# Optimization experiments

Measured on AMD Instinct MI355X. Metric: run time of the kernel, lower is better.

The kernel has to match this reference:

```python
import jax, jax.numpy as jnp
import numpy as np

B, L, P = 65536, 512, 96
E_LIN, E = 14, 16
FFT = 512
TEMP = 0.07
K = 2
EPS = 1e-5


def setup_inputs() -> dict:
    key = jax.random.key(0)
    k0, k1, k2 = jax.random.split(key, 3)
    x = jax.random.normal(k0, (B, L), dtype=jnp.float32)
    Wg = jax.random.normal(k1, (E, FFT // 2), dtype=jnp.float32) * 0.02
    bg = jnp.zeros((E,), dtype=jnp.float32)
    Wr = jax.random.normal(k2, (E_LIN, P, L), dtype=jnp.float32) * 0.02
    br = jnp.zeros((E_LIN, P), dtype=jnp.float32)
    return {"x": x, "Wg": Wg, "bg": bg, "Wr": Wr, "br": br}


def _periodogram(x):
    # x: [B, L] -> normalized power spectrum [B, FFT//2]
    x0 = x - jnp.mean(x, axis=1, keepdims=True)
    dft = jnp.fft.fft(x0, n=FFT, axis=1) / np.float32(np.sqrt(FFT))
    dft = dft[:, : FFT // 2]
    I = dft.real ** 2 + dft.imag ** 2
    s = jnp.sum(I, axis=1, keepdims=True)
    s = jnp.where(s == 0, jnp.ones_like(s), s)
    return I / s


def reference(x, Wg, bg, Wr, br):
    # gating (eval mode: no noise, divide by temperature)
    I = _periodogram(x)                                  # [B, F/2]
    gate = (I @ Wg.T + bg) / TEMP                        # [B, E]
    topv, topi = jax.lax.top_k(gate, K)                  # [B, K]
    gates = jax.nn.softmax(topv, axis=1)                 # [B, K]

    # RLinear experts: RevIN(norm) -> Linear -> RevIN(denorm); stats detached
    mu = jax.lax.stop_gradient(jnp.mean(x, axis=1, keepdims=True))        # [B,1]
    sd = jax.lax.stop_gradient(jnp.sqrt(jnp.var(x, axis=1, keepdims=True) + EPS))
    xn = (x - mu) / sd                                   # [B, L]
    yr = jnp.einsum('bl,epl->bep', xn, Wr) + br          # [B, E_LIN, P]
    yr = yr * sd[:, :, None] + mu[:, :, None]

    mean_out = jnp.broadcast_to(jnp.mean(x, axis=1, keepdims=True), (x.shape[0], P))[:, None, :]
    naive_out = jnp.broadcast_to(x[:, -1:], (x.shape[0], P))[:, None, :]

    eo = jnp.concatenate([yr, mean_out, naive_out], axis=1)   # [B, E, P]
    sel = jnp.take_along_axis(eo, topi[:, :, None], axis=1)   # [B, K, P]
    out = jnp.sum(gates[:, :, None] * sel, axis=1)            # [B, P]
    return out
```

## Files before the change

kernel.cpp:

```cpp
#include <hip/hip_runtime.h>
#include <math.h>

#define NB_B 65536
#define NL   512
#define NP   96
#define NE   16
#define NEL  14
#define NF   256
#define TEMP_INV (1.0f/0.07f)
#define TAU  1e-5f
#define PI_D 3.14159265358979323846
#define MAXCHK 1536

typedef __attribute__((ext_vector_type(8))) short bf16x8;
typedef __attribute__((ext_vector_type(4))) float f32x4;


#define WS_PCNT     0
#define WS_HOLES    16384
#define WS_PBASE    32768
#define WS_FLAGCNT  33792
#define WS_NCHK     33824
#define WS_HOLECNT  33840
#define WS_FLAG     33856
#define WS_SSUM     296000
#define WS_WGT      301376
#define WS_BGT      317760
#define WS_TWD      319872
#define WS_REC      328064
#define WS_HDR      590208
#define WS_RIDX     1638784
#define WS_WRB      1900928
#define WS_DESC     3473792
#define WS_XB16     3480064
#define WS_WRBF     70588928
#define WS_WRBF_END 72161792

__device__ __forceinline__ unsigned short f2bf(float f) {
    unsigned u = __float_as_uint(f);
    unsigned r = (u + 0x7fffu + ((u >> 16) & 1u)) >> 16;
    return (unsigned short)r;
}

__global__ __launch_bounds__(256) void k_prep(
    const float* __restrict__ Wg, const float* __restrict__ bg,
    const float* __restrict__ Wr,
    float* __restrict__ Ssum, float* __restrict__ WgE, float* __restrict__ bgT,
    double2* __restrict__ twd,
    int* __restrict__ pcnt, int* __restrict__ flagcnt, int* __restrict__ holecnt,
    ushort4* __restrict__ Wrb, ushort4* __restrict__ WrbF, int perm)
{
    int g = blockIdx.x * 256 + threadIdx.x;
    {
        ushort4 o = make_ushort4(0, 0, 0, 0);
        if (g < NEL * NP * NL / 4) {
            float4 v;
            if (perm) {
                int row = g >> 7, sq = g & 127;
                int ll = sq >> 1, kb = (sq & 1) * 4;
                const float* wr = Wr + (size_t)row * NL + ll;
                v.x = wr[(kb + 0) * 64]; v.y = wr[(kb + 1) * 64];
                v.z = wr[(kb + 2) * 64]; v.w = wr[(kb + 3) * 64];
            } else {
                v = ((const float4*)Wr)[g];
            }
            o.x = f2bf(v.x); o.y = f2bf(v.y); o.z = f2bf(v.z); o.w = f2bf(v.w);
        }
        Wrb[g] = o;
    }
    if (WrbF) {
        ushort4 o = make_ushort4(0, 0, 0, 0);
        int idx  = g >> 1;
        int lane = idx & 63;
        int idx2 = idx >> 6;
        int nt   = idx2 % 6;
        int idx3 = idx2 / 6;
        int ks   = idx3 & 1;
        int idx4 = idx3 >> 1;
        int kb8  = idx4 & 7;
        int e    = idx4 >> 3;
        if (e < NEL) {
            int p = nt * 16 + (lane & 15);
            int quad = lane >> 4;
            int skb = kb8 * 64 + ks * 32 + quad * 8 + (g & 1) * 4;
            const float* wr = Wr + ((size_t)e * NP + p) * NL;
            float vv[4];
#pragma unroll
            for (int jj = 0; jj < 4; jj++) {
                int sk = skb + jj;
                int ko = perm ? ((sk & 7) * 64 + (sk >> 3)) : sk;
                vv[jj] = wr[ko];
            }
            o.x = f2bf(vv[0]); o.y = f2bf(vv[1]); o.z = f2bf(vv[2]); o.w = f2bf(vv[3]);
        }
        WrbF[g] = o;
    }
    if (g < NEL * NP * 8) {
        int row = g >> 3, seg = g & 7;
        const float4* w = (const float4*)(Wr + (size_t)row * NL + seg * 64);
        float s = 0.f;
#pragma unroll
        for (int i = 0; i < 16; i++) { float4 v = w[i]; s += v.x + v.y + v.z + v.w; }
        s += __shfl_xor(s, 1); s += __shfl_xor(s, 2); s += __shfl_xor(s, 4);
        if (seg == 0) Ssum[row] = s;
    }
    if (g < 4096) {
        int c = g & 3, e = (g >> 2) & 15, f4 = g >> 6;
        WgE[g] = Wg[e * NF + f4 * 4 + c] * TEMP_INV;
    }
    if (g < 512) {
        double a = -2.0 * PI_D * (double)g / 512.0;
        twd[g] = make_double2(cos(a), sin(a));
    }
    if (g < 256) pcnt[g << 4] = 0;
    if (g < NE) bgT[g] = bg[g] * TEMP_INV;
    if (g == 300) *flagcnt = 0;
    if (g == 301) *holecnt = 0;
}

__global__ __launch_bounds__(256) void k_gate(
    const float* __restrict__ x,
    const float4* __restrict__ WgE4, const float* __restrict__ bgT,
    int* __restrict__ rec, float4* __restrict__ hdr,
    int* __restrict__ flaglist, int* __restrict__ flagcnt,
    int* __restrict__ pcnt, unsigned short* __restrict__ xb16)
{
    __shared__ __align__(16) float2 s_z[4][576];
    float* s_Iv = (float*)&s_z[0][0];

    const int t = threadIdx.x;
    const int wv = t >> 6, l = t & 63;
    const int b0 = blockIdx.x * 8 + wv * 2;

    const float th = -6.283185307179586f / 512.0f;
    const float R2 = 0.70710678118654752f;
    float s1, c1; __sincosf((float)l * th, &s1, &c1);
    float s2, c2; __sincosf((float)(2 * l) * th, &s2, &c2);
    float sw0, cw0; __sincosf((float)((l & 31) << 3) * th, &sw0, &cw0);
    float sw1, cw1; __sincosf((float)((l & 15) << 4) * th, &sw1, &cw1);
    float sw2, cw2; __sincosf((float)((l & 7) << 5) * th, &sw2, &cw2);
    float2 tw0[4];
    tw0[0] = make_float2(c1, s1);
    tw0[1] = make_float2(R2 * (c1 + s1), R2 * (s1 - c1));
    tw0[2] = make_float2(s1, -c1);
    tw0[3] = make_float2(tw0[1].y, -tw0[1].x);
    float2 tw1[2];
    tw1[0] = make_float2(c2, s2);
    tw1[1] = make_float2(s2, -c2);
    const float2 w2 = make_float2(c2 * c2 - s2 * s2, 2.f * c2 * s2);
    float2 wst[5];
    wst[0] = make_float2(cw0, sw0);
    wst[1] = make_float2(cw1, sw1);
    wst[2] = make_float2(cw2, sw2);
    {
        int j2 = l & 3;
        float cc3 = (j2 == 0) ? 1.f : (j2 == 1) ? R2 : (j2 == 2) ? 0.f : -R2;
        float ss3 = (j2 == 0) ? 0.f : (j2 == 2) ? -1.f : -R2;
        wst[3] = make_float2(cc3, ss3);
    }
    wst[4] = (l & 1) ? make_float2(0.f, -1.f) : make_float2(1.f, 0.f);

    const float* xa = x + (size_t)b0 * NL;
    const float* xb = xa + NL;
    float xr[8], xi[8];
#pragma unroll
    for (int k = 0; k < 8; k++) { xr[k] = xa[k * 64 + l]; xi[k] = xb[k * 64 + l]; }
    const float last_a = __shfl(xr[7], 63);
    const float last_b = __shfl(xi[7], 63);

    if (xb16) {
        unsigned pa_[4], pb_[4];
#pragma unroll
        for (int j = 0; j < 4; j++) {
            asm("v_cvt_pk_bf16_f32 %0, %1, %2" : "=v"(pa_[j]) : "v"(xr[2 * j]), "v"(xr[2 * j + 1]));
            asm("v_cvt_pk_bf16_f32 %0, %1, %2" : "=v"(pb_[j]) : "v"(xi[2 * j]), "v"(xi[2 * j + 1]));
        }
        *(uint4*)(xb16 + (size_t)b0 * NL + l * 8)       = *(uint4*)pa_;
        *(uint4*)(xb16 + (size_t)(b0 + 1) * NL + l * 8) = *(uint4*)pb_;
    }

#pragma unroll
    for (int k = 0; k < 4; k++) {
        float2 w = tw0[k];
        float ur = xr[k], ui = xi[k], vr = xr[k + 4], vi = xi[k + 4];
        xr[k] = ur + vr; xi[k] = ui + vi;
        float dr = ur - vr, di = ui - vi;
        xr[k + 4] = dr * w.x - di * w.y; xi[k + 4] = dr * w.y + di * w.x;
    }
    {
        const int kk[4] = {0, 1, 4, 5};
#pragma unroll
        for (int g2 = 0; g2 < 4; g2++) {
            int k = kk[g2];
            float2 w = tw1[k & 1];
            float ur = xr[k], ui = xi[k], vr = xr[k + 2], vi = xi[k + 2];
            xr[k] = ur + vr; xi[k] = ui + vi;
            float dr = ur - vr, di = ui - vi;
            xr[k + 2] = dr * w.x - di * w.y; xi[k + 2] = dr * w.y + di * w.x;
        }
    }
    {
#pragma unroll
        for (int k = 0; k < 8; k += 2) {
            float ur = xr[k], ui = xi[k], vr = xr[k + 1], vi = xi[k + 1];
            xr[k] = ur + vr; xi[k] = ui + vi;
            float dr = ur - vr, di = ui - vi;
            xr[k + 1] = dr * w2.x - di * w2.y; xi[k + 1] = dr * w2.y + di * w2.x;
        }
    }
#pragma unroll
    for (int st = 3; st < 8; st++) {
        const int half = 256 >> st;
        const float2 w = wst[st - 3];
        const bool up = (l & half) != 0;
        const float sg = up ? -1.f : 1.f;
        const float cc = up ? w.x : 1.f;
        const float ss = up ? w.y : 0.f;
#pragma unroll
        for (int k = 0; k < 8; k++) {
            float pr = __shfl_xor(xr[k], half);
            float pi = __shfl_xor(xi[k], half);
            float tr = fmaf(sg, xr[k], pr);
            float ti = fmaf(sg, xi[k], pi);
            xr[k] = tr * cc - ti * ss;
            xi[k] = tr * ss + ti * cc;
        }
    }
    {
        const float sg = (l & 1) ? -1.f : 1.f;
#pragma unroll
        for (int k = 0; k < 8; k++) {
            float pr = __shfl_xor(xr[k], 1);
            float pi = __shfl_xor(xi[k], 1);
            xr[k] = fmaf(sg, xr[k], pr);
            xi[k] = fmaf(sg, xi[k], pi);
        }
    }

#pragma unroll
    for (int k = 0; k < 8; k++) {
        int i = k * 64 + l;
        s_z[wv][i + (i >> 3)] = make_float2(xr[k], xi[k]);
    }

    float Ia[4], Ib[4];
    float psa = 0.f, psb = 0.f;
#pragma unroll
    for (int j = 0; j < 4; j++) {
        int f = (l << 2) | j;
        int i1_ = (int)(__brev((unsigned)f) >> 23);
        int i2_ = (int)(__brev((unsigned)((512 - f) & 511)) >> 23);
        float2 z1 = s_z[wv][i1_ + (i1_ >> 3)];
        float2 z2 = s_z[wv][i2_ + (i2_ >> 3)];
        float pr_ = z1.x + z2.x, qm = z1.y - z2.y;
        float qp = z1.y + z2.y, pm = z1.x - z2.x;
        float va = pr_ * pr_ + qm * qm;
        float vb = qp * qp + pm * pm;
        if (f == 0) { va = 0.f; vb = 0.f; }
        Ia[j] = va; Ib[j] = vb;
        psa += va; psb += vb;
    }
#pragma unroll
    for (int m = 1; m < 64; m <<= 1) {
        psa += __shfl_xor(psa, m); psb += __shfl_xor(psb, m);
    }
    const float psa_raw = psa, psb_raw = psb;
    if (psa == 0.f) psa = 1.f;
    if (psb == 0.f) psb = 1.f;
    const float inv_a = 1.f / psa, inv_b = 1.f / psb;

    const float2 Z0   = s_z[wv][0];
    const float2 Z256 = s_z[wv][1];

    float* wI = s_Iv + wv * 1152;
    const int io = (l << 2) + ((l >> 4) << 2);
    *(float4*)(wI + io)       = make_float4(Ia[0], Ia[1], Ia[2], Ia[3]);
    *(float4*)(wI + 272 + io) = make_float4(Ib[0], Ib[1], Ib[2], Ib[3]);

    const int e16 = l & 15, cq = l >> 4;
    const float bgv = bgT[e16];
    float accA = 0.f, accB = 0.f;
    const float* rA = wI + cq * 68;
    const float* rB = rA + 272;
#pragma unroll 4
    for (int jj = 0; jj < 16; jj++) {
        float4 ia = *(const float4*)(rA + 4 * jj);
        float4 ib = *(const float4*)(rB + 4 * jj);
        float4 w = WgE4[(cq * 16 + jj) * 16 + e16];
        accA += ia.x * w.x + ia.y * w.y + ia.z * w.z + ia.w * w.w;
        accB += ib.x * w.x + ib.y * w.y + ib.z * w.z + ib.w * w.w;
    }
    accA += __shfl_xor(accA, 16); accA += __shfl_xor(accA, 32);
    accB += __shfl_xor(accB, 16); accB += __shfl_xor(accB, 32);

    float v = ((l & 16) ? accB * inv_b : accA * inv_a) + bgv;

    float b0v = v; int b0i = e16;
#pragma unroll
    for (int m = 1; m < 16; m <<= 1) {
        float ov = __shfl_xor(b0v, m); int oi = __shfl_xor(b0i, m);
        if (ov > b0v || (ov == b0v && oi < b0i)) { b0v = ov; b0i = oi; }
    }
    float v1 = (e16 == b0i) ? -1e30f : v;
    float b1v = v1; int b1i = e16;
#pragma unroll
    for (int m = 1; m < 16; m <<= 1) {
        float ov = __shfl_xor(b1v, m); int oi = __shfl_xor(b1i, m);
        if (ov > b1v || (ov == b1v && oi < b1i)) { b1v = ov; b1i = oi; }
    }
    float v2 = (e16 == b1i) ? -1e30f : v1;
    float b2v = v2;
#pragma unroll
    for (int m = 1; m < 16; m <<= 1) {
        float ov = __shfl_xor(b2v, m);
        b2v = fmaxf(b2v, ov);
    }

    if (l == 0 || l == 16) {
        const int r = l >> 4;
        const int b = b0 + r;
        const float mu = (r ? Z0.y : Z0.x) * (1.f / 512.f);
        const float Jv = r ? Z256.y : Z256.x;
        const float ps = r ? psb_raw : psa_raw;
        const float sd = sqrtf((0.5f * ps + Jv * Jv) * (1.f / 262144.f) + 1e-5f);
        const float last = r ? last_b : last_a;
        const float w0 = 1.f / (1.f + expf(b1v - b0v));
        const int pid = b0i * 16 + b1i;
        const int lo = atomicAdd(&pcnt[pid << 4], 1);
        rec[b] = (pid << 24) | lo;
        hdr[b] = make_float4(mu, sd, last, w0);
        if (b1v - b2v < TAU) {
            int pos = atomicAdd(flagcnt, 1);
            flaglist[pos] = b;
        }
    }
}

__global__ __launch_bounds__(256) void k_refine(
    const float* __restrict__ x, const double2* __restrict__ twd,
    const float* __restrict__ Wg, const float* __restrict__ bg,
    int* __restrict__ rec, float4* __restrict__ hdr,
    const int* __restrict__ flaglist, const int* __restrict__ flagcnt,
    int* __restrict__ pcnt, int* __restrict__ holes, int* __restrict__ holecnt)
{
    __shared__ double s_x[512];
    __shared__ double s_I[256];
    __shared__ double s_red[16];
    __shared__ double s_g[16];
    const int nf = *flagcnt;
    const int t = threadIdx.x;
    const int wid = t >> 6, lane = t & 63;
    for (int fi = blockIdx.x; fi < nf; fi += gridDim.x) {
        const int b = flaglist[fi];
        const float* xp = x + (size_t)b * NL;
        double v0 = (double)xp[t], v1 = (double)xp[t + 256];
        double lsum = v0 + v1;
        for (int m = 1; m < 64; m <<= 1) lsum += __shfl_xor(lsum, m);
        if (lane == 0) s_red[wid] = lsum;
        __syncthreads();
        double mu = (s_red[0] + s_red[1] + s_red[2] + s_red[3]) * (1.0 / 512.0);
        s_x[t] = v0 - mu; s_x[t + 256] = v1 - mu;
        __syncthreads();
        double2 w = twd[t];
        double pr = 1.0, pi = 0.0, cr = 0.0, ci = 0.0;
        for (int n = 0; n < 512; n++) {
            double xv = s_x[n];
            cr += xv * pr; ci += xv * pi;
            double t2 = pr * w.x - pi * w.y;
            pi = pr * w.y + pi * w.x;
            pr = t2;
        }
        double I = cr * cr + ci * ci;
        s_I[t] = I;
        double ls = I;
        for (int m = 1; m < 64; m <<= 1) ls += __shfl_xor(ls, m);
        if (lane == 0) s_red[8 + wid] = ls;
        __syncthreads();
        double stot = s_red[8] + s_red[9] + s_red[10] + s_red[11];
        if (stot == 0.0) stot = 1.0;
        if (t < 16) {
            double acc = 0.0;
            const float* wrow = Wg + t * NF;
            for (int f = 0; f < NF; f++) acc += s_I[f] * (double)wrow[f];
            s_g[t] = (acc / stot + (double)bg[t]) * (1.0 / 0.07);
        }
        __syncthreads();
        if (t == 0) {
            double c0 = -1e300, c1 = -1e300; int j0 = 0, j1 = 0;
            for (int i = 0; i < 16; i++) {
                double v = s_g[i];
                if (v > c0) { c1 = c0; j1 = j0; c0 = v; j0 = i; }
                else if (v > c1) { c1 = v; j1 = i; }
            }
            double e1 = exp(c1 - c0);
            float w0f = (float)(1.0 / (1.0 + e1));
            int newpid = j0 * 16 + j1;
            int oldrec = rec[b];
            int oldpid = (int)(((unsigned)oldrec) >> 24);
            if (newpid == oldpid) {
                ((float*)(hdr + b))[3] = w0f;
            } else {
                int pos = atomicAdd(holecnt, 1);
                if (pos < 4096) {
                    int nlo = atomicAdd(&pcnt[newpid << 4], 1);
                    rec[b] = (newpid << 24) | nlo;
                    holes[pos] = oldrec;
                    ((float*)(hdr + b))[3] = w0f;
                }
            }
        }
        __syncthreads();
    }
}

__global__ __launch_bounds__(256) void k_scan(
    const int* __restrict__ pcnt, int* __restrict__ pbase,
    int* __restrict__ desc, int* __restrict__ nchk)
{
    __shared__ int s[256], c[256];
    const int t = threadIdx.x;
    const int n = pcnt[t << 4];
    s[t] = n;
    c[t] = (n + 63) >> 6;
    __syncthreads();
    for (int off = 1; off < 256; off <<= 1) {
        int v1 = (t >= off) ? s[t - off] : 0;
        int v2 = (t >= off) ? c[t - off] : 0;
        __syncthreads();
        s[t] += v1; c[t] += v2;
        __syncthreads();
    }
    int excl = t ? s[t - 1] : 0;
    int cexcl = t ? c[t - 1] : 0;
    pbase[t] = excl;
    int myc = (n + 63) >> 6;
    for (int j = 0; j < myc; j++) desc[cexcl + j] = (t << 16) | j;
    if (t == 255) *nchk = cexcl + myc;
}

__global__ __launch_bounds__(256) void k_scatter(
    const int* __restrict__ rec, const int* __restrict__ pbase,
    int* __restrict__ ridx,
    const int* __restrict__ holes, const int* __restrict__ holecnt)
{
    const int t = threadIdx.x;
    const int b = blockIdx.x * 256 + t;
    unsigned v = (unsigned)rec[b];
    ridx[pbase[v >> 24] + (v & 0xFFFFFF)] = b;
    if (blockIdx.x == 0) {
        int nh = *holecnt; if (nh > 4096) nh = 4096;
        for (int h = t; h < nh; h += 256) {
            unsigned hv = (unsigned)holes[h];
            ridx[pbase[hv >> 24] + (hv & 0xFFFFFF)] = -1;
        }
    }
}

__global__ __launch_bounds__(256) void k_gemm_reg(
    const unsigned short* __restrict__ xb16,
    const unsigned short* __restrict__ WrbF,
    const float* __restrict__ br, const float* __restrict__ Ssum,
    const float4* __restrict__ hdr, float* __restrict__ out,
    const int* __restrict__ pcnt, const int* __restrict__ pbase,
    const int* __restrict__ ridx,
    const int* __restrict__ desc, const int* __restrict__ nchk)
{
    __shared__ int    s_idx[64];
    __shared__ float4 s_hdr[64];
    __shared__ float  s_br[2][96], s_S[2][96];
    if ((int)blockIdx.x >= *nchk) return;
    const int d = desc[blockIdx.x];
    const int pid = d >> 16, cc = d & 0xffff;
    const int n = pcnt[pid << 4];
    const int base = pbase[pid];
    const int i0 = pid >> 4, i1 = pid & 15;
    const int t = threadIdx.x;
    const int lane = t & 63, wv = t >> 6;
    const int quad = lane >> 4, l16 = lane & 15;
    if (t < 96) {
        s_br[0][t] = (i0 < NEL) ? br[i0 * NP + t] : 0.f;
        s_S [0][t] = (i0 < NEL) ? Ssum[i0 * NP + t] : 0.f;
        s_br[1][t] = (i1 < NEL) ? br[i1 * NP + t] : 0.f;
        s_S [1][t] = (i1 < NEL) ? Ssum[i1 * NP + t] : 0.f;
    }
    if (t < 64) {
        int g = cc * 64 + t;
        bool vld = g < n;
        int row = vld ? ridx[base + g] : -1;
        s_idx[t] = row;
        s_hdr[t] = (row >= 0) ? hdr[row] : make_float4(0.f, 0.f, 0.f, 0.f);
    }
    __syncthreads();

    int myrow = s_idx[wv * 16 + l16]; if (myrow < 0) myrow = 0;
    const unsigned short* aP = xb16 + (size_t)myrow * NL + quad * 8;
    const unsigned short* bP[2];
    bP[0] = WrbF + (size_t)i0 * 49152 + lane * 8;
    bP[1] = WrbF + (size_t)i1 * 49152 + lane * 8;

    f32x4 acc[2][6];
#pragma unroll
    for (int ex = 0; ex < 2; ex++)
#pragma unroll
        for (int j = 0; j < 6; j++) acc[ex][j] = (f32x4){0.f, 0.f, 0.f, 0.f};

#pragma unroll
    for (int kb8 = 0; kb8 < 8; kb8++) {
        bf16x8 a0 = *(const bf16x8*)(aP + kb8 * 64);
        bf16x8 a1 = *(const bf16x8*)(aP + kb8 * 64 + 32);
        bf16x8 bfr[2][2][6];
#pragma unroll
        for (int ks = 0; ks < 2; ks++)
#pragma unroll
            for (int ex = 0; ex < 2; ex++)
#pragma unroll
                for (int nt = 0; nt < 6; nt++)
                    bfr[ks][ex][nt] = *(const bf16x8*)(bP[ex] + kb8 * 6144 + ks * 3072 + nt * 512);
#pragma unroll
        for (int ks = 0; ks < 2; ks++)
#pragma unroll
            for (int ex = 0; ex < 2; ex++)
#pragma unroll
                for (int nt = 0; nt < 6; nt++)
                    acc[ex][nt] = __builtin_amdgcn_mfma_f32_16x16x32_bf16(
                        ks ? a1 : a0, bfr[ks][ex][nt], acc[ex][nt], 0, 0, 0);
    }

#pragma unroll
    for (int i = 0; i < 4; i++) {
        int rloc = wv * 16 + quad * 4 + i;
        int row = s_idx[rloc];
        if (row >= 0) {
            float4 h = s_hdr[rloc];
            float mu = h.x, sd = h.y, last = h.z, w0 = h.w, w1 = 1.f - w0;
            float* orow = out + (size_t)row * NP;
#pragma unroll
            for (int nt = 0; nt < 6; nt++) {
                int p = nt * 16 + l16;
                float v0 = (i0 < NEL) ? (mu + s_br[0][p] * sd - mu * s_S[0][p] + acc[0][nt][i])
                                      : (i0 == NEL ? mu : last);
                float v1 = (i1 < NEL) ? (mu + s_br[1][p] * sd - mu * s_S[1][p] + acc[1][nt][i])
                                      : (i1 == NEL ? mu : last);
                orow[p] = w0 * v0 + w1 * v1;
            }
        }
    }
}

template<int XB>
__global__ __launch_bounds__(256) void k_gemm(
    const float* __restrict__ x, const unsigned short* __restrict__ xb16,
    const unsigned short* __restrict__ Wrb,
    const float* __restrict__ br, const float* __restrict__ Ssum,
    const float4* __restrict__ hdr, float* __restrict__ out,
    const int* __restrict__ pcnt, const int* __restrict__ pbase,
    const int* __restrict__ ridx,
    const int* __restrict__ desc, const int* __restrict__ nchk)
{
    __shared__ __align__(16) unsigned short sA[64 * 72];
    __shared__ __align__(16) unsigned short sB[2][96 * 72];
    __shared__ int    s_idx[64];
    __shared__ float4 s_hdr[64];
    __shared__ float  s_br[2][96], s_S[2][96];
    if ((int)blockIdx.x >= *nchk) return;
    const int d = desc[blockIdx.x];
    const int pid = d >> 16, cc = d & 0xffff;
    const int n = pcnt[pid << 4];
    const int base = pbase[pid];
    const int i0 = pid >> 4, i1 = pid & 15;
    const int t = threadIdx.x;
    const int lane = t & 63, wv = t >> 6;
    const int quad = lane >> 4, l16 = lane & 15;
    const int ar = t >> 2, asub = t & 3;
    if (t < 96) {
        s_br[0][t] = (i0 < NEL) ? br[i0 * NP + t] : 0.f;
        s_S [0][t] = (i0 < NEL) ? Ssum[i0 * NP + t] : 0.f;
        s_br[1][t] = (i1 < NEL) ? br[i1 * NP + t] : 0.f;
        s_S [1][t] = (i1 < NEL) ? Ssum[i1 * NP + t] : 0.f;
    }
    if (t < 64) {
        int g = cc * 64 + t;
        bool vld = g < n;
        int row = vld ? ridx[base + g] : -1;
        s_idx[t] = row;
        s_hdr[t] = (row >= 0) ? hdr[row] : make_float4(0.f, 0.f, 0.f, 0.f);
    }
    __syncthreads();

    f32x4 acc[2][6];
#pragma unroll
    for (int ex = 0; ex < 2; ex++)
#pragma unroll
        for (int j = 0; j < 6; j++) acc[ex][j] = (f32x4){0.f, 0.f, 0.f, 0.f};

    int rr = s_idx[ar]; if (rr < 0) rr = 0;

    unsigned boff[6];
    unsigned short* bdst[6];
    const unsigned short* wb[2];
    wb[0] = Wrb + (size_t)i0 * NP * NL;
    wb[1] = Wrb + (size_t)i1 * NP * NL;
    int bex[6];
#pragma unroll
    for (int it = 0; it < 6; it++) {
        int ex = (it >= 3);
        int fl = t + (it - 3 * ex) * 256;
        int p = fl >> 3, kg = fl & 7;
        bex[it] = ex;
        boff[it] = (unsigned)(p * NL + kg * 8);
        bdst[it] = &sB[ex][p * 72 + kg * 8];
    }
    unsigned short* adst = sA + ar * 72 + asub * 16;

    const unsigned short* xrow16 = xb16 + (size_t)rr * NL + asub * 16;
    const float* xrowf = x + (size_t)rr * NL + asub * 16;

    bf16x8 aR[2]; float4 fA[4]; bf16x8 bR[6];

    if constexpr (XB) {
        aR[0] = *(const bf16x8*)(xrow16);
        aR[1] = *(const bf16x8*)(xrow16 + 8);
    } else {
#pragma unroll
        for (int i = 0; i < 4; i++) fA[i] = ((const float4*)xrowf)[i];
    }
#pragma unroll
    for (int it = 0; it < 6; it++) bR[it] = *(const bf16x8*)(wb[bex[it]] + boff[it]);

    for (int kb = 0; kb < NL; kb += 64) {
        if constexpr (XB) {
            *(bf16x8*)adst       = aR[0];
            *(bf16x8*)(adst + 8) = aR[1];
        } else {
            unsigned short tmp[16];
#pragma unroll
            for (int i = 0; i < 4; i++) {
                float4 v = fA[i];
                tmp[i * 4 + 0] = f2bf(v.x); tmp[i * 4 + 1] = f2bf(v.y);
                tmp[i * 4 + 2] = f2bf(v.z); tmp[i * 4 + 3] = f2bf(v.w);
            }
            *(bf16x8*)adst       = *(bf16x8*)tmp;
            *(bf16x8*)(adst + 8) = *(bf16x8*)(tmp + 8);
        }
#pragma unroll
        for (int it = 0; it < 6; it++) *(bf16x8*)bdst[it] = bR[it];
        __syncthreads();

        const int kn = kb + 64;
        if (kn < NL) {
            if constexpr (XB) {
                aR[0] = *(const bf16x8*)(xrow16 + kn);
                aR[1] = *(const bf16x8*)(xrow16 + kn + 8);
            } else {
#pragma unroll
                for (int i = 0; i < 4; i++) fA[i] = ((const float4*)(xrowf + kn))[i];
            }
#pragma unroll
            for (int it = 0; it < 6; it++)
                bR[it] = *(const bf16x8*)(wb[bex[it]] + boff[it] + kn);
        }

#pragma unroll
        for (int ks = 0; ks < 2; ks++) {
            bf16x8 af = *(const bf16x8*)(sA + (wv * 16 + l16) * 72 + ks * 32 + quad * 8);
#pragma unroll
            for (int ex = 0; ex < 2; ex++)
#pragma unroll
                for (int nt = 0; nt < 6; nt++) {
                    bf16x8 bf = *(const bf16x8*)(&sB[ex][(nt * 16 + l16) * 72 + ks * 32 + quad * 8]);
                    acc[ex][nt] = __builtin_amdgcn_mfma_f32_16x16x32_bf16(af, bf, acc[ex][nt], 0, 0, 0);
                }
        }
        __syncthreads();
    }
#pragma unroll
    for (int i = 0; i < 4; i++) {
        int rloc = wv * 16 + quad * 4 + i;
        int row = s_idx[rloc];
        if (row >= 0) {
            float4 h = s_hdr[rloc];
            float mu = h.x, sd = h.y, last = h.z, w0 = h.w, w1 = 1.f - w0;
            float* orow = out + (size_t)row * NP;
#pragma unroll
            for (int nt = 0; nt < 6; nt++) {
                int p = nt * 16 + l16;
                float v0 = (i0 < NEL) ? (mu + s_br[0][p] * sd - mu * s_S[0][p] + acc[0][nt][i])
                                      : (i0 == NEL ? mu : last);
                float v1 = (i1 < NEL) ? (mu + s_br[1][p] * sd - mu * s_S[1][p] + acc[1][nt][i])
                                      : (i1 == NEL ? mu : last);
                orow[p] = w0 * v0 + w1 * v1;
            }
        }
    }
}

extern "C" void kernel_launch(void* const* d_in, const int* in_sizes, int n_in,
                              void* d_out, int out_size, void* d_ws, size_t ws_size,
                              hipStream_t stream)
{
    const float* x  = (const float*)d_in[0];
    const float* Wg = (const float*)d_in[1];
    const float* bg = (const float*)d_in[2];
    const float* Wr = (const float*)d_in[3];
    const float* br = (const float*)d_in[4];
    float* out = (float*)d_out;
    char* ws = (char*)d_ws;

    int*     pcnt     = (int*)(ws + WS_PCNT);
    int*     holes    = (int*)(ws + WS_HOLES);
    int*     pbase    = (int*)(ws + WS_PBASE);
    int*     flagcnt  = (int*)(ws + WS_FLAGCNT);
    int*     nchk     = (int*)(ws + WS_NCHK);
    int*     holecnt  = (int*)(ws + WS_HOLECNT);
    int*     flaglist = (int*)(ws + WS_FLAG);
    float*   Ssum     = (float*)(ws + WS_SSUM);
    float*   WgE      = (float*)(ws + WS_WGT);
    float*   bgT      = (float*)(ws + WS_BGT);
    double2* twd      = (double2*)(ws + WS_TWD);
    int*     rec      = (int*)(ws + WS_REC);
    float4*  hdr      = (float4*)(ws + WS_HDR);
    int*     ridx     = (int*)(ws + WS_RIDX);
    unsigned short* Wrb = (unsigned short*)(ws + WS_WRB);
    int*     desc     = (int*)(ws + WS_DESC);

    const int use_xb  = (ws_size >= (size_t)WS_WRBF);
    const int use_xb2 = (ws_size >= (size_t)WS_WRBF_END);
    unsigned short* xb16 = use_xb  ? (unsigned short*)(ws + WS_XB16) : (unsigned short*)0;
    unsigned short* WrbF = use_xb2 ? (unsigned short*)(ws + WS_WRBF) : (unsigned short*)0;

    k_prep<<<dim3(768), dim3(256), 0, stream>>>(Wg, bg, Wr, Ssum, WgE, bgT, twd,
                                                pcnt, flagcnt, holecnt,
                                                (ushort4*)Wrb, (ushort4*)WrbF, use_xb);
    k_gate<<<dim3(NB_B / 8), dim3(256), 0, stream>>>(x, (const float4*)WgE, bgT,
                                                     rec, hdr, flaglist, flagcnt, pcnt, xb16);
    k_refine<<<dim3(512), dim3(256), 0, stream>>>(x, twd, Wg, bg, rec, hdr,
                                                  flaglist, flagcnt, pcnt, holes, holecnt);
    k_scan<<<dim3(1), dim3(256), 0, stream>>>(pcnt, pbase, desc, nchk);
    k_scatter<<<dim3(NB_B / 256), dim3(256), 0, stream>>>(rec, pbase, ridx, holes, holecnt);
    if (use_xb2)
        k_gemm_reg<<<dim3(MAXCHK), dim3(256), 0, stream>>>(xb16, WrbF, br, Ssum, hdr, out,
                                                           pcnt, pbase, ridx, desc, nchk);
    else if (use_xb)
        k_gemm<1><<<dim3(MAXCHK), dim3(256), 0, stream>>>(x, xb16, Wrb, br, Ssum, hdr, out,
                                                          pcnt, pbase, ridx, desc, nchk);
    else
        k_gemm<0><<<dim3(MAXCHK), dim3(256), 0, stream>>>(x, xb16, Wrb, br, Ssum, hdr, out,
                                                          pcnt, pbase, ridx, desc, nchk);
}
```

Measured before the change: 311.9 us.

## Stage expert weights through double-buffered LDS and split gate launch

Drops the fragment-ordered WrbF weight copy. The GEMM kernel now stages both experts' bf16 weight tiles through a double-buffered shared-memory buffer (stride 68) and reads A fragments directly from the bf16 copy of x in global memory, prefetching the next K block while MFMAs run. The gate kernel gains a launch-bounds occupancy hint and is split into two half-grid launches using a block offset. The aim is to cut per-block global weight traffic and remove the weight-permutation work in prep, at the cost of extra LDS use and one barrier per K step.

```diff
diff --git a/kernel.cpp b/kernel.cpp
--- a/kernel.cpp
+++ b/kernel.cpp
@@ -30,11 +30,10 @@
 #define WS_REC      328064
 #define WS_HDR      590208
 #define WS_RIDX     1638784
-#define WS_WRB      1900928
-#define WS_DESC     3473792
-#define WS_XB16     3480064
-#define WS_WRBF     70588928
-#define WS_WRBF_END 72161792
+#define WS_WRB      1933696
+#define WS_DESC     3506560
+#define WS_XB16     3512704
+#define WS_XB16_END 70621568
 
 __device__ __forceinline__ unsigned short f2bf(float f) {
     unsigned u = __float_as_uint(f);
@@ -48,7 +47,7 @@
     float* __restrict__ Ssum, float* __restrict__ WgE, float* __restrict__ bgT,
     double2* __restrict__ twd,
     int* __restrict__ pcnt, int* __restrict__ flagcnt, int* __restrict__ holecnt,
-    ushort4* __restrict__ Wrb, ushort4* __restrict__ WrbF, int perm)
+    ushort4* __restrict__ Wrb, int perm)
 {
     int g = blockIdx.x * 256 + threadIdx.x;
     {
@@ -68,33 +67,6 @@
         }
         Wrb[g] = o;
     }
-    if (WrbF) {
-        ushort4 o = make_ushort4(0, 0, 0, 0);
-        int idx  = g >> 1;
-        int lane = idx & 63;
-        int idx2 = idx >> 6;
-        int nt   = idx2 % 6;
-        int idx3 = idx2 / 6;
-        int ks   = idx3 & 1;
-        int idx4 = idx3 >> 1;
-        int kb8  = idx4 & 7;
-        int e    = idx4 >> 3;
-        if (e < NEL) {
-            int p = nt * 16 + (lane & 15);
-            int quad = lane >> 4;
-            int skb = kb8 * 64 + ks * 32 + quad * 8 + (g & 1) * 4;
-            const float* wr = Wr + ((size_t)e * NP + p) * NL;
-            float vv[4];
-#pragma unroll
-            for (int jj = 0; jj < 4; jj++) {
-                int sk = skb + jj;
-                int ko = perm ? ((sk & 7) * 64 + (sk >> 3)) : sk;
-                vv[jj] = wr[ko];
-            }
-            o.x = f2bf(vv[0]); o.y = f2bf(vv[1]); o.z = f2bf(vv[2]); o.w = f2bf(vv[3]);
-        }
-        WrbF[g] = o;
-    }
     if (g < NEL * NP * 8) {
         int row = g >> 3, seg = g & 7;
         const float4* w = (const float4*)(Wr + (size_t)row * NL + seg * 64);
@@ -118,19 +90,19 @@
     if (g == 301) *holecnt = 0;
 }
 
-__global__ __launch_bounds__(256) void k_gate(
+__global__ __launch_bounds__(256, 4) void k_gate(
     const float* __restrict__ x,
     const float4* __restrict__ WgE4, const float* __restrict__ bgT,
     int* __restrict__ rec, float4* __restrict__ hdr,
     int* __restrict__ flaglist, int* __restrict__ flagcnt,
-    int* __restrict__ pcnt, unsigned short* __restrict__ xb16)
+    int* __restrict__ pcnt, unsigned short* __restrict__ xb16, int bofs)
 {
     __shared__ __align__(16) float2 s_z[4][576];
     float* s_Iv = (float*)&s_z[0][0];
 
     const int t = threadIdx.x;
     const int wv = t >> 6, l = t & 63;
-    const int b0 = blockIdx.x * 8 + wv * 2;
+    const int b0 = (bofs + blockIdx.x) * 8 + wv * 2;
 
     const float th = -6.283185307179586f / 512.0f;
     const float R2 = 0.70710678118654752f;
@@ -456,15 +428,16 @@
     }
 }
 
-__global__ __launch_bounds__(256) void k_gemm_reg(
+__global__ __launch_bounds__(256) void k_gemm2(
     const unsigned short* __restrict__ xb16,
-    const unsigned short* __restrict__ WrbF,
+    const unsigned short* __restrict__ Wrb,
     const float* __restrict__ br, const float* __restrict__ Ssum,
     const float4* __restrict__ hdr, float* __restrict__ out,
     const int* __restrict__ pcnt, const int* __restrict__ pbase,
     const int* __restrict__ ridx,
     const int* __restrict__ desc, const int* __restrict__ nchk)
 {
+    __shared__ __align__(16) unsigned short sB[2][2][96 * 68];
     __shared__ int    s_idx[64];
     __shared__ float4 s_hdr[64];
     __shared__ float  s_br[2][96], s_S[2][96];
@@ -490,13 +463,30 @@
         s_idx[t] = row;
         s_hdr[t] = (row >= 0) ? hdr[row] : make_float4(0.f, 0.f, 0.f, 0.f);
     }
+
+    const unsigned short* wb[2];
+    wb[0] = Wrb + (size_t)i0 * NP * NL;
+    wb[1] = Wrb + (size_t)i1 * NP * NL;
+    unsigned boff[6]; int bpos[6], bex[6];
+#pragma unroll
+    for (int it = 0; it < 6; it++) {
+        int ex = (it >= 3);
+        int fl = t + (it - 3 * ex) * 256;
+        int p = fl >> 3, kg = fl & 7;
+        bex[it] = ex;
+        boff[it] = (unsigned)(p * NL + kg * 8);
+        bpos[it] = p * 68 + kg * 8;
+    }
+
+    bf16x8 bR[6];
+#pragma unroll
+    for (int it = 0; it < 6; it++) bR[it] = *(const bf16x8*)(wb[bex[it]] + boff[it]);
+#pragma unroll
+    for (int it = 0; it < 6; it++) *(bf16x8*)(&sB[0][bex[it]][bpos[it]]) = bR[it];
     __syncthreads();
 
-    int myrow = s_idx[wv * 16 + l16]; if (myrow < 0) myrow = 0;
-    const unsigned short* aP = xb16 + (size_t)myrow * NL + quad * 8;
-    const unsigned short* bP[2];
-    bP[0] = WrbF + (size_t)i0 * 49152 + lane * 8;
-    bP[1] = WrbF + (size_t)i1 * 49152 + lane * 8;
+    int arow = s_idx[wv * 16 + l16]; if (arow < 0) arow = 0;
+    const unsigned short* aP = xb16 + (size_t)arow * NL + quad * 8;
 
     f32x4 acc[2][6];
 #pragma unroll
@@ -504,26 +494,37 @@
 #pragma unroll
         for (int j = 0; j < 6; j++) acc[ex][j] = (f32x4){0.f, 0.f, 0.f, 0.f};
 
-#pragma unroll
-    for (int kb8 = 0; kb8 < 8; kb8++) {
-        bf16x8 a0 = *(const bf16x8*)(aP + kb8 * 64);
-        bf16x8 a1 = *(const bf16x8*)(aP + kb8 * 64 + 32);
-        bf16x8 bfr[2][2][6];
+    bf16x8 a0 = *(const bf16x8*)(aP);
+    bf16x8 a1 = *(const bf16x8*)(aP + 32);
+
+    int cb = 0;
+    for (int kb = 0; kb < NL; kb += 64) {
+        const int kn = kb + 64;
+        bf16x8 an0, an1;
+        if (kn < NL) {
+#pragma unroll
+            for (int it = 0; it < 6; it++)
+                bR[it] = *(const bf16x8*)(wb[bex[it]] + boff[it] + kn);
+            an0 = *(const bf16x8*)(aP + kn);
+            an1 = *(const bf16x8*)(aP + kn + 32);
+        }
 #pragma unroll
         for (int ks = 0; ks < 2; ks++)
 #pragma unroll
             for (int ex = 0; ex < 2; ex++)
 #pragma unroll
-                for (int nt = 0; nt < 6; nt++)
-                    bfr[ks][ex][nt] = *(const bf16x8*)(bP[ex] + kb8 * 6144 + ks * 3072 + nt * 512);
-#pragma unroll
-        for (int ks = 0; ks < 2; ks++)
-#pragma unroll
-            for (int ex = 0; ex < 2; ex++)
-#pragma unroll
-                for (int nt = 0; nt < 6; nt++)
+                for (int nt = 0; nt < 6; nt++) {
+                    bf16x8 bf = *(const bf16x8*)(&sB[cb][ex][(nt * 16 + l16) * 68 + ks * 32 + quad * 8]);
                     acc[ex][nt] = __builtin_amdgcn_mfma_f32_16x16x32_bf16(
-                        ks ? a1 : a0, bfr[ks][ex][nt], acc[ex][nt], 0, 0, 0);
+                        ks ? a1 : a0, bf, acc[ex][nt], 0, 0, 0);
+                }
+        if (kn < NL) {
+#pragma unroll
+            for (int it = 0; it < 6; it++) *(bf16x8*)(&sB[cb ^ 1][bex[it]][bpos[it]]) = bR[it];
+            __syncthreads();
+            cb ^= 1;
+            a0 = an0; a1 = an1;
+        }
     }
 
 #pragma unroll
@@ -547,9 +548,8 @@
     }
 }
 
-template<int XB>
-__global__ __launch_bounds__(256) void k_gemm(
-    const float* __restrict__ x, const unsigned short* __restrict__ xb16,
+__global__ __launch_bounds__(256) void k_gemm_f32(
+    const float* __restrict__ x,
     const unsigned short* __restrict__ Wrb,
     const float* __restrict__ br, const float* __restrict__ Ssum,
     const float4* __restrict__ hdr, float* __restrict__ out,
@@ -611,50 +611,32 @@
         bdst[it] = &sB[ex][p * 72 + kg * 8];
     }
     unsigned short* adst = sA + ar * 72 + asub * 16;
-
-    const unsigned short* xrow16 = xb16 + (size_t)rr * NL + asub * 16;
     const float* xrowf = x + (size_t)rr * NL + asub * 16;
 
-    bf16x8 aR[2]; float4 fA[4]; bf16x8 bR[6];
-
-    if constexpr (XB) {
-        aR[0] = *(const bf16x8*)(xrow16);
-        aR[1] = *(const bf16x8*)(xrow16 + 8);
-    } else {
-#pragma unroll
-        for (int i = 0; i < 4; i++) fA[i] = ((const float4*)xrowf)[i];
-    }
+    float4 fA[4]; bf16x8 bR[6];
+#pragma unroll
+    for (int i = 0; i < 4; i++) fA[i] = ((const float4*)xrowf)[i];
 #pragma unroll
     for (int it = 0; it < 6; it++) bR[it] = *(const bf16x8*)(wb[bex[it]] + boff[it]);
 
     for (int kb = 0; kb < NL; kb += 64) {
-        if constexpr (XB) {
-            *(bf16x8*)adst       = aR[0];
-            *(bf16x8*)(adst + 8) = aR[1];
-        } else {
-            unsigned short tmp[16];
-#pragma unroll
-            for (int i = 0; i < 4; i++) {
-                float4 v = fA[i];
-                tmp[i * 4 + 0] = f2bf(v.x); tmp[i * 4 + 1] = f2bf(v.y);
-                tmp[i * 4 + 2] = f2bf(v.z); tmp[i * 4 + 3] = f2bf(v.w);
-            }
-            *(bf16x8*)adst       = *(bf16x8*)tmp;
-            *(bf16x8*)(adst + 8) = *(bf16x8*)(tmp + 8);
-        }
+        unsigned short tmp[16];
+#pragma unroll
+        for (int i = 0; i < 4; i++) {
+            float4 v = fA[i];
+            tmp[i * 4 + 0] = f2bf(v.x); tmp[i * 4 + 1] = f2bf(v.y);
+            tmp[i * 4 + 2] = f2bf(v.z); tmp[i * 4 + 3] = f2bf(v.w);
+        }
+        *(bf16x8*)adst       = *(bf16x8*)tmp;
+        *(bf16x8*)(adst + 8) = *(bf16x8*)(tmp + 8);
 #pragma unroll
         for (int it = 0; it < 6; it++) *(bf16x8*)bdst[it] = bR[it];
         __syncthreads();
 
         const int kn = kb + 64;
         if (kn < NL) {
-            if constexpr (XB) {
-                aR[0] = *(const bf16x8*)(xrow16 + kn);
-                aR[1] = *(const bf16x8*)(xrow16 + kn + 8);
-            } else {
-#pragma unroll
-                for (int i = 0; i < 4; i++) fA[i] = ((const float4*)(xrowf + kn))[i];
-            }
+#pragma unroll
+            for (int i = 0; i < 4; i++) fA[i] = ((const float4*)(xrowf + kn))[i];
 #pragma unroll
             for (int it = 0; it < 6; it++)
                 bR[it] = *(const bf16x8*)(wb[bex[it]] + boff[it] + kn);
@@ -723,27 +705,26 @@
     unsigned short* Wrb = (unsigned short*)(ws + WS_WRB);
     int*     desc     = (int*)(ws + WS_DESC);
 
-    const int use_xb  = (ws_size >= (size_t)WS_WRBF);
-    const int use_xb2 = (ws_size >= (size_t)WS_WRBF_END);
-    unsigned short* xb16 = use_xb  ? (unsigned short*)(ws + WS_XB16) : (unsigned short*)0;
-    unsigned short* WrbF = use_xb2 ? (unsigned short*)(ws + WS_WRBF) : (unsigned short*)0;
+    const int use_xb = (ws_size >= (size_t)WS_XB16_END);
+    unsigned short* xb16 = use_xb ? (unsigned short*)(ws + WS_XB16) : (unsigned short*)0;
 
     k_prep<<<dim3(768), dim3(256), 0, stream>>>(Wg, bg, Wr, Ssum, WgE, bgT, twd,
                                                 pcnt, flagcnt, holecnt,
-                                                (ushort4*)Wrb, (ushort4*)WrbF, use_xb);
-    k_gate<<<dim3(NB_B / 8), dim3(256), 0, stream>>>(x, (const float4*)WgE, bgT,
-                                                     rec, hdr, flaglist, flagcnt, pcnt, xb16);
+                                                (ushort4*)Wrb, use_xb);
+    k_gate<<<dim3(NB_B / 16), dim3(256), 0, stream>>>(x, (const float4*)WgE, bgT,
+                                                      rec, hdr, flaglist, flagcnt, pcnt,
+                                                      xb16, 0);
+    k_gate<<<dim3(NB_B / 16), dim3(256), 0, stream>>>(x, (const float4*)WgE, bgT,
+                                                      rec, hdr, flaglist, flagcnt, pcnt,
+                                                      xb16, NB_B / 16);
     k_refine<<<dim3(512), dim3(256), 0, stream>>>(x, twd, Wg, bg, rec, hdr,
                                                   flaglist, flagcnt, pcnt, holes, holecnt);
     k_scan<<<dim3(1), dim3(256), 0, stream>>>(pcnt, pbase, desc, nchk);
     k_scatter<<<dim3(NB_B / 256), dim3(256), 0, stream>>>(rec, pbase, ridx, holes, holecnt);
-    if (use_xb2)
-        k_gemm_reg<<<dim3(MAXCHK), dim3(256), 0, stream>>>(xb16, WrbF, br, Ssum, hdr, out,
+    if (use_xb)
+        k_gemm2<<<dim3(MAXCHK), dim3(256), 0, stream>>>(xb16, Wrb, br, Ssum, hdr, out,
+                                                        pcnt, pbase, ridx, desc, nchk);
+    else
+        k_gemm_f32<<<dim3(MAXCHK), dim3(256), 0, stream>>>(x, Wrb, br, Ssum, hdr, out,
                                                            pcnt, pbase, ridx, desc, nchk);
-    else if (use_xb)
-        k_gemm<1><<<dim3(MAXCHK), dim3(256), 0, stream>>>(x, xb16, Wrb, br, Ssum, hdr, out,
-                                                          pcnt, pbase, ridx, desc, nchk);
-    else
-        k_gemm<0><<<dim3(MAXCHK), dim3(256), 0, stream>>>(x, xb16, Wrb, br, Ssum, hdr, out,
-                                                          pcnt, pbase, ridx, desc, nchk);
-}
+}
```

Result: no change. 306.7 us (-1.7%).
